# Performance work log

Measured on AMD Instinct MI355X. Metric: run time of the kernel, lower is better.

## Reference

```python
import jax, jax.numpy as jnp
import numpy as np

D_MODEL = 512
D_STATE = 64
SEQ_LEN = 8192
BATCH = 8
LN_EPS = 1e-3  # keras LayerNormalization default epsilon
DELTA_MIN = 0.001
DELTA_MAX = 0.8 * (2.0 / D_STATE)  # default when use_hippo_init=True


def setup_inputs() -> dict:
    key = jax.random.key(0)
    ks = jax.random.split(key, 10)
    x = jax.random.normal(ks[0], (BATCH, SEQ_LEN, D_MODEL), dtype=jnp.float32)
    # Dense layers: glorot-uniform-ish init via scaled normal for simplicity
    def dense_w(k, fan_in, fan_out):
        lim = np.sqrt(6.0 / (fan_in + fan_out))
        return jax.random.uniform(k, (fan_in, fan_out), minval=-lim, maxval=lim, dtype=jnp.float32)
    W_in = dense_w(ks[1], D_MODEL, D_MODEL)
    b_in = jnp.zeros((D_MODEL,), jnp.float32)
    W_xs = dense_w(ks[2], D_MODEL, D_STATE)
    # HiPPO-LegS log init: A_log = log(n+1)
    A_log = jnp.log(jnp.arange(1, D_STATE + 1, dtype=jnp.float32))
    log_delta = jax.random.uniform(ks[3], (D_STATE,), minval=np.log(DELTA_MIN), maxval=np.log(DELTA_MAX), dtype=jnp.float32)
    B = jnp.ones((D_STATE,), jnp.float32)
    C = jax.random.normal(ks[4], (D_STATE,), dtype=jnp.float32)  # stddev=1.0
    D = jnp.ones((D_MODEL,), jnp.float32)
    W_so = dense_w(ks[5], D_STATE, D_MODEL)
    W_out = dense_w(ks[6], D_MODEL, D_MODEL)
    b_out = jnp.zeros((D_MODEL,), jnp.float32)
    ln_gamma = jnp.ones((D_MODEL,), jnp.float32)
    ln_beta = jnp.zeros((D_MODEL,), jnp.float32)
    return {
        "x": x, "ln_gamma": ln_gamma, "ln_beta": ln_beta,
        "W_in": W_in, "b_in": b_in, "W_xs": W_xs,
        "A_log": A_log, "log_delta": log_delta, "B": B, "C": C, "D": D,
        "W_so": W_so, "W_out": W_out, "b_out": b_out,
    }


def reference(x, ln_gamma, ln_beta, W_in, b_in, W_xs, A_log, log_delta, B, C, D, W_so, W_out, b_out):
    Bsz, L, dm = x.shape
    n_fft = 1 << int(np.ceil(np.log2(2 * L - 1)))
    residual = x
    # LayerNorm over last axis (keras default)
    mu = jnp.mean(x, axis=-1, keepdims=True)
    var = jnp.mean(jnp.square(x - mu), axis=-1, keepdims=True)
    xn = (x - mu) * jax.lax.rsqrt(var + LN_EPS) * ln_gamma + ln_beta
    z = xn @ W_in + b_in                       # (B, L, d_model)
    x_state = z @ W_xs                          # (B, L, d_state)
    # Diagonal SSM discretization (bilinear/Tustin)
    A = -jnp.exp(A_log)
    delta = jax.nn.softplus(log_delta)
    dA2 = delta * A / 2.0
    A_bar = (1.0 + dA2) / (1.0 - dA2)           # (d_state,)
    B_bar = delta / (1.0 - dA2) * B             # (d_state,)
    t = jnp.arange(L, dtype=jnp.float32)
    kernel = jnp.power(A_bar[None, :], t[:, None]) * B_bar[None, :]  # (L, d_state)
    # FFT convolution along time
    u_t = jnp.transpose(x_state, (0, 2, 1))     # (B, d_state, L)
    k_t = kernel.T                              # (d_state, L)
    u_f = jnp.fft.rfft(u_t, n=n_fft, axis=-1)
    k_f = jnp.fft.rfft(k_t, n=n_fft, axis=-1)
    y = jnp.fft.irfft(u_f * k_f[None, :, :], n=n_fft, axis=-1)[:, :, :L]
    y_state = jnp.transpose(y, (0, 2, 1))       # (B, L, d_state)
    y_state = y_state * C[None, None, :]
    y = y_state @ W_so                          # (B, L, d_model)
    y = y + D * z
    y = y @ W_out + b_out
    return y + residual
```

## Files before the change

kernel.cpp:

```cpp
#include <hip/hip_runtime.h>
#include <hip/hip_bf16.h>
#include <cstddef>
#include <cstdint>

#define DM 512
#define DS 64
#define L_SEQ 8192
#define NB 8
#define M_ROWS (NB * L_SEQ)
#define LN_EPS 1e-3f
#define NCHUNK 256
#define LCH 32

typedef __attribute__((ext_vector_type(8))) short short8;
typedef __attribute__((ext_vector_type(4))) float f32x4;
using bf16 = __hip_bfloat16;
using ushort_t = unsigned short;

__device__ __forceinline__ unsigned short f2bf(float f) {
    bf16 h = __float2bfloat16(f);
    return *reinterpret_cast<unsigned short*>(&h);
}

__device__ __forceinline__ int swzcol(int row, int col) {
    return (col & ~63) | (((((col >> 3) & 7) ^ (row & 7))) << 3) | (col & 7);
}

__device__ __forceinline__ size_t pkidx(int k, int n, int Kd32) {
    int n16 = n >> 4, fr = n & 15, kt = k >> 5, fq = (k >> 3) & 3, e = k & 7;
    return (((size_t)(n16 * Kd32 + kt) * 64 + fq * 16 + fr) << 3) + e;
}

__device__ __forceinline__ void gload_lds16(const void* g, void* l) {
    __builtin_amdgcn_global_load_lds(
        (const __attribute__((address_space(1))) void*)g,
        (__attribute__((address_space(3))) void*)l, 16, 0, 0);
}

template<int N> __device__ __forceinline__ void wait_vm() {
    static_assert(N == 0 || N == 6, "");
    if constexpr (N == 0) asm volatile("s_waitcnt vmcnt(0)" ::: "memory");
    else                  asm volatile("s_waitcnt vmcnt(6)" ::: "memory");
}

__device__ __forceinline__ void block_barrier() {
    asm volatile("" ::: "memory");
    __builtin_amdgcn_s_barrier();
    asm volatile("" ::: "memory");
}

__global__ __launch_bounds__(256) void prep(const float* __restrict__ W_so,
                                            const float* __restrict__ W_out,
                                            const float* __restrict__ W_in,
                                            const float* __restrict__ W_xs,
                                            const float* __restrict__ b_in,
                                            float* __restrict__ sWsoOut,
                                            float* __restrict__ sWinxs,
                                            float* __restrict__ sBxs)
{
    int i = blockIdx.x * 256 + threadIdx.x;
    if (i < 32768) {
        int s = i >> 9, j = i & 511;
        float a = 0.f;
        for (int c = 0; c < 512; ++c) a += W_so[s * 512 + c] * W_out[c * 512 + j];
        sWsoOut[i] = a;
    } else if (i < 65536) {
        int idx = i - 32768; int k = idx >> 6, n = idx & 63;
        float a = 0.f;
        for (int c = 0; c < 512; ++c) a += W_in[k * 512 + c] * W_xs[c * 64 + n];
        sWinxs[idx] = a;
    } else if (i < 65600) {
        int n = i - 65536;
        float a = 0.f;
        for (int c = 0; c < 512; ++c) a += b_in[c] * W_xs[c * 64 + n];
        sBxs[n] = a;
    }
}

__global__ __launch_bounds__(256) void pack_all(const float* __restrict__ W_in,
                                                const float* __restrict__ sWinxs,
                                                const float* __restrict__ sWsoOut,
                                                const float* __restrict__ W_out,
                                                const float* __restrict__ Dv,
                                                ushort_t* __restrict__ WinPk,
                                                ushort_t* __restrict__ WinxsPk,
                                                ushort_t* __restrict__ WsooutPk,
                                                ushort_t* __restrict__ WdoutPk)
{
    int i = blockIdx.x * 256 + threadIdx.x;
    if (i < 262144) {
        int k = i >> 9, n = i & 511;
        WinPk[pkidx(k, n, 16)] = f2bf(W_in[i]);
    } else if (i < 294912) {
        int j = i - 262144; int k = j >> 6, n = j & 63;
        WinxsPk[pkidx(k, n, 16)] = f2bf(sWinxs[j]);
    } else if (i < 327680) {
        int j = i - 294912; int s = j >> 9, n = j & 511;
        WsooutPk[pkidx(s, n, 2)] = f2bf(sWsoOut[j]);
    } else if (i < 589824) {
        int j = i - 327680; int c = j >> 9, n = j & 511;
        WdoutPk[pkidx(c, n, 16)] = f2bf(Dv[c] * W_out[j]);
    }
}

__global__ __launch_bounds__(64) void ln_kernel(const float* __restrict__ x,
                                                const float* __restrict__ gamma,
                                                const float* __restrict__ beta,
                                                ushort_t* __restrict__ xn)
{
    size_t row = blockIdx.x;
    int lane = threadIdx.x;
    const float4* xr = (const float4*)(x + row * DM);
    float4 v0 = xr[lane * 2];
    float4 v1 = xr[lane * 2 + 1];
    float s  = v0.x + v0.y + v0.z + v0.w + v1.x + v1.y + v1.z + v1.w;
    float s2 = v0.x*v0.x + v0.y*v0.y + v0.z*v0.z + v0.w*v0.w
             + v1.x*v1.x + v1.y*v1.y + v1.z*v1.z + v1.w*v1.w;
    #pragma unroll
    for (int off = 32; off > 0; off >>= 1) {
        s  += __shfl_xor(s,  off);
        s2 += __shfl_xor(s2, off);
    }
    float mu  = s * (1.0f / DM);
    float var = s2 * (1.0f / DM) - mu * mu;
    float rs  = rsqrtf(var + LN_EPS);
    const float4* g4 = (const float4*)gamma;
    const float4* b4 = (const float4*)beta;
    float4 g0 = g4[lane * 2], g1 = g4[lane * 2 + 1];
    float4 bb0 = b4[lane * 2], bb1 = b4[lane * 2 + 1];
    short8 o;
    o[0] = (short)f2bf((v0.x - mu) * rs * g0.x + bb0.x);
    o[1] = (short)f2bf((v0.y - mu) * rs * g0.y + bb0.y);
    o[2] = (short)f2bf((v0.z - mu) * rs * g0.z + bb0.z);
    o[3] = (short)f2bf((v0.w - mu) * rs * g0.w + bb0.w);
    o[4] = (short)f2bf((v1.x - mu) * rs * g1.x + bb1.x);
    o[5] = (short)f2bf((v1.y - mu) * rs * g1.y + bb1.y);
    o[6] = (short)f2bf((v1.z - mu) * rs * g1.z + bb1.z);
    o[7] = (short)f2bf((v1.w - mu) * rs * g1.w + bb1.w);
    int g = (lane & 7) ^ ((int)row & 7);
    *(short8*)(xn + row * DM + (lane >> 3) * 64 + g * 8) = o;
}

__device__ __forceinline__ void store_out(float* C, size_t i, float v) { C[i] = v; }
__device__ __forceinline__ void store_out(bf16* C, size_t i, float v)  { C[i] = __float2bfloat16(v); }

template<int BN, int WR, int WC, typename OutT, bool DUAL, bool HB, bool HA, bool SWZO>
__global__ __launch_bounds__(512, 4) void gemm_bp(const ushort_t* __restrict__ A1,
                                                  const ushort_t* __restrict__ B1,
                                                  const ushort_t* __restrict__ A2,
                                                  const ushort_t* __restrict__ B2,
                                                  const float* __restrict__ bias,
                                                  const float* __restrict__ aux,
                                                  OutT* __restrict__ C,
                                                  int M, int N, int K2)
{
    constexpr int BM = 128;
    constexpr int MF = BM / (16 * WR), NF = BN / (16 * WC);
    static_assert(NF == 2, "b ping-pong arrays assume NF==2");
    __shared__ unsigned char LDS[2][BM * 128];

    const int tid = threadIdx.x;
    const int lane = tid & 63, w = tid >> 6;
    const int fr = lane & 15, fq = lane >> 4;
    const int wr = w % WR, wc = w / WR;

    const int ny = N / BN;
    const int per = (int)gridDim.x >> 3;
    const int lg = ((int)blockIdx.x & 7) * per + ((int)blockIdx.x >> 3);
    const size_t bm0 = (size_t)(lg / ny) * BM;
    const int bn0 = (lg % ny) * BN;
    const int nk = (DUAL ? 1 : 0) + K2 / 64;

    f32x4 acc[MF][NF];
    #pragma unroll
    for (int m = 0; m < MF; ++m)
        #pragma unroll
        for (int n = 0; n < NF; ++n)
            acc[m][n] = (f32x4){0.f, 0.f, 0.f, 0.f};

    auto stage = [&](int buf, int t) {
        #pragma unroll
        for (int j = 0; j < 2; ++j) {
            int r = j * 64 + (tid >> 3);
            const ushort_t* src;
            if constexpr (DUAL) {
                if (t == 0) src = A1 + (bm0 + r) * (size_t)64 + (tid & 7) * 8;
                else        src = A2 + (bm0 + r) * (size_t)512 + (size_t)(t - 1) * 64 + (tid & 7) * 8;
            } else {
                src = A2 + (bm0 + r) * (size_t)K2 + (size_t)t * 64 + (tid & 7) * 8;
            }
            gload_lds16(src, &LDS[buf][j * 8192 + w * 1024]);
        }
    };

    auto loadB = [&](short8 (&bb)[2][2], int t) {
        #pragma unroll
        for (int h = 0; h < 2; ++h)
            #pragma unroll
            for (int n = 0; n < NF; ++n) {
                int n16g = (bn0 + wc * (BN / WC) + n * 16) >> 4;
                const ushort_t* p;
                if constexpr (DUAL) {
                    if (t == 0) p = B1 + (((size_t)(n16g * 2 + h) * 64 + lane) << 3);
                    else        p = B2 + (((size_t)(n16g * 16 + (t - 1) * 2 + h) * 64 + lane) << 3);
                } else {
                    p = B2 + (((size_t)(n16g * (K2 / 32) + t * 2 + h) * 64 + lane) << 3);
                }
                bb[h][n] = *(const short8*)p;
            }
    };

    auto compute = [&](int buf, const short8 (&bb)[2][2]) {
        #pragma unroll
        for (int h = 0; h < 2; ++h) {
            short8 af[MF];
            #pragma unroll
            for (int m = 0; m < MF; ++m) {
                int row = wr * (BM / WR) + m * 16 + fr;
                int g = (h * 4 + fq) ^ (row & 7);
                af[m] = *(const short8*)&LDS[buf][row * 128 + g * 16];
            }
            #pragma unroll
            for (int m = 0; m < MF; ++m)
                #pragma unroll
                for (int n = 0; n < NF; ++n)
                    acc[m][n] = __builtin_amdgcn_mfma_f32_16x16x32_bf16(af[m], bb[h][n], acc[m][n], 0, 0, 0);
        }
    };

    short8 bX[2][2], bY[2][2];
    stage(0, 0);
    loadB(bX, 0);
    int buf = 0;
    for (int t = 0; t < nk; t += 2) {
        if (t + 1 < nk) { stage(buf ^ 1, t + 1); loadB(bY, t + 1); }
        __builtin_amdgcn_sched_barrier(0);
        if (t + 1 < nk) wait_vm<6>(); else wait_vm<0>();
        block_barrier();
        compute(buf, bX);
        if (t + 1 < nk) {
            block_barrier();
            buf ^= 1;
            if (t + 2 < nk) { stage(buf ^ 1, t + 2); loadB(bX, t + 2); }
            __builtin_amdgcn_sched_barrier(0);
            if (t + 2 < nk) wait_vm<6>(); else wait_vm<0>();
            block_barrier();
            compute(buf, bY);
            if (t + 2 < nk) { block_barrier(); buf ^= 1; }
        }
    }

    #pragma unroll
    for (int n = 0; n < NF; ++n) {
        int coll = wc * (BN / WC) + n * 16 + fr;
        int colg = bn0 + coll;
        float bv = HB ? bias[colg] : 0.f;
        #pragma unroll
        for (int m = 0; m < MF; ++m) {
            int rowl = wr * (BM / WR) + m * 16 + fq * 4;
            #pragma unroll
            for (int r = 0; r < 4; ++r) {
                size_t row = bm0 + rowl + r;
                float v = acc[m][n][r] + bv;
                if constexpr (HA) v += aux[row * (size_t)N + colg];
                size_t oc = SWZO ? (size_t)swzcol(rowl + r, colg) : (size_t)colg;
                store_out(C, row * (size_t)N + oc, v);
            }
        }
    }
}

__device__ __forceinline__ void ssm_params(const float* A_log, const float* log_delta,
                                           const float* Bv, int n, float& Ab, float& Bb)
{
    float A  = -expf(A_log[n]);
    float dl = log1pf(expf(log_delta[n]));
    float dA2 = dl * A * 0.5f;
    float inv = 1.0f / (1.0f - dA2);
    Ab = (1.0f + dA2) * inv;
    Bb = dl * inv * Bv[n];
}

__global__ __launch_bounds__(64) void scan_pass1(const float* __restrict__ xs,
                                                 const float* __restrict__ A_log,
                                                 const float* __restrict__ log_delta,
                                                 const float* __restrict__ Bv,
                                                 float* __restrict__ carry)
{
    int b = blockIdx.x / NCHUNK;
    int c = blockIdx.x % NCHUNK;
    int n = threadIdx.x;
    float Ab, Bb;
    ssm_params(A_log, log_delta, Bv, n, Ab, Bb);
    size_t base = ((size_t)b * L_SEQ + (size_t)c * LCH) * DS + n;
    float h = 0.0f;
    for (int t = 0; t < LCH; ++t)
        h = Ab * h + Bb * xs[base + (size_t)t * DS];
    carry[((size_t)b * NCHUNK + c) * DS + n] = h;
}

__global__ __launch_bounds__(64) void scan_pass2(const float* __restrict__ A_log,
                                                 const float* __restrict__ log_delta,
                                                 const float* __restrict__ Bv,
                                                 const float* __restrict__ carry,
                                                 float* __restrict__ hin)
{
    int b = blockIdx.x;
    int n = threadIdx.x;
    float Ab, Bb;
    ssm_params(A_log, log_delta, Bv, n, Ab, Bb);
    float powA = powf(Ab, (float)LCH);
    float h = 0.0f;
    for (int c = 0; c < NCHUNK; ++c) {
        size_t idx = ((size_t)b * NCHUNK + c) * DS + n;
        hin[idx] = h;
        h = powA * h + carry[idx];
    }
}

__global__ __launch_bounds__(64) void scan_pass3(const float* __restrict__ xs,
                                                 const float* __restrict__ A_log,
                                                 const float* __restrict__ log_delta,
                                                 const float* __restrict__ Bv,
                                                 const float* __restrict__ Cv,
                                                 const float* __restrict__ hin,
                                                 ushort_t* __restrict__ ys)
{
    int b = blockIdx.x / NCHUNK;
    int c = blockIdx.x % NCHUNK;
    int n = threadIdx.x;
    float Ab, Bb;
    ssm_params(A_log, log_delta, Bv, n, Ab, Bb);
    float Cn = Cv[n];
    size_t base = ((size_t)b * L_SEQ + (size_t)c * LCH) * DS + n;
    size_t rowbase = ((size_t)b * L_SEQ + (size_t)c * LCH) * DS;
    float h = hin[((size_t)b * NCHUNK + c) * DS + n];
    for (int t = 0; t < LCH; ++t) {
        h = Ab * h + Bb * xs[base + (size_t)t * DS];
        int col = (((n >> 3) ^ (t & 7)) << 3) | (n & 7);
        ys[rowbase + (size_t)t * DS + col] = f2bf(Cn * h);
    }
}

extern "C" void kernel_launch(void* const* d_in, const int* in_sizes, int n_in,
                              void* d_out, int out_size, void* d_ws, size_t ws_size,
                              hipStream_t stream)
{
    const float* x         = (const float*)d_in[0];
    const float* ln_gamma  = (const float*)d_in[1];
    const float* ln_beta   = (const float*)d_in[2];
    const float* W_in      = (const float*)d_in[3];
    const float* b_in      = (const float*)d_in[4];
    const float* W_xs      = (const float*)d_in[5];
    const float* A_log     = (const float*)d_in[6];
    const float* log_delta = (const float*)d_in[7];
    const float* Bv        = (const float*)d_in[8];
    const float* Cv        = (const float*)d_in[9];
    const float* Dv        = (const float*)d_in[10];
    const float* W_so      = (const float*)d_in[11];
    const float* W_out     = (const float*)d_in[12];
    const float* b_out     = (const float*)d_in[13];
    float* out = (float*)d_out;

    const size_t M = M_ROWS;
    float*    xs_f     = (float*)d_ws;
    ushort_t* xn_b     = (ushort_t*)(xs_f + M * DS);
    ushort_t* z_b      = xn_b + M * (size_t)DM;
    ushort_t* ys_b     = z_b + M * (size_t)DM;
    ushort_t* WinPk    = ys_b + M * (size_t)DS;
    ushort_t* WinxsPk  = WinPk + (size_t)DM * DM;
    ushort_t* WsooutPk = WinxsPk + (size_t)DM * DS;
    ushort_t* WdoutPk  = WsooutPk + (size_t)DS * DM;
    float*    sWsoOut  = (float*)(WdoutPk + (size_t)DM * DM);
    float*    sWinxs   = sWsoOut + (size_t)DS * DM;
    float*    sBxs     = sWinxs + (size_t)DM * DS;
    float*    carry    = sBxs + 64;
    float*    hin      = carry + NB * NCHUNK * DS;

    prep<<<dim3(257), dim3(256), 0, stream>>>(W_so, W_out, W_in, W_xs, b_in,
                                              sWsoOut, sWinxs, sBxs);
    pack_all<<<dim3(589824 / 256), dim3(256), 0, stream>>>(W_in, sWinxs, sWsoOut, W_out, Dv,
                                                           WinPk, WinxsPk, WsooutPk, WdoutPk);
    ln_kernel<<<dim3((unsigned)M), dim3(64), 0, stream>>>(x, ln_gamma, ln_beta, xn_b);
    gemm_bp<128, 2, 4, bf16, false, true, false, true>
        <<<dim3((M / 128) * (DM / 128)), dim3(512), 0, stream>>>(nullptr, nullptr, xn_b, WinPk,
                                                                 b_in, nullptr, (bf16*)z_b,
                                                                 (int)M, DM, DM);
    gemm_bp<64, 4, 2, float, false, true, false, false>
        <<<dim3(M / 128), dim3(512), 0, stream>>>(nullptr, nullptr, xn_b, WinxsPk,
                                                  sBxs, nullptr, xs_f, (int)M, DS, DM);
    scan_pass1<<<dim3(NB * NCHUNK), dim3(64), 0, stream>>>(xs_f, A_log, log_delta, Bv, carry);
    scan_pass2<<<dim3(NB), dim3(64), 0, stream>>>(A_log, log_delta, Bv, carry, hin);
    scan_pass3<<<dim3(NB * NCHUNK), dim3(64), 0, stream>>>(xs_f, A_log, log_delta, Bv, Cv, hin, ys_b);
    gemm_bp<128, 2, 4, float, true, true, true, false>
        <<<dim3((M / 128) * (DM / 128)), dim3(512), 0, stream>>>(ys_b, WsooutPk, z_b, WdoutPk,
                                                                 b_out, x, out, (int)M, DM, DM);
}
```

Before: 259.0 us.

## Fold W_in·diag(D)·W_out into one weight, drop the z GEMM and its buffer

Precomputes W_in·diag(D)·W_out and a combined bias so the final GEMM reads the normalized input directly rather than the intermediate z. This removes the full M×512×512 input-projection GEMM and the bf16 write and read of z. In exchange, the prep kernel gains a per-call 512×512×512 weight product on naive scalar loops, plus extra bf16 rounding of the fused weights.

```diff
diff --git a/kernel.cpp b/kernel.cpp
--- a/kernel.cpp
+++ b/kernel.cpp
@@ -54,52 +54,60 @@
                                             const float* __restrict__ W_in,
                                             const float* __restrict__ W_xs,
                                             const float* __restrict__ b_in,
-                                            float* __restrict__ sWsoOut,
-                                            float* __restrict__ sWinxs,
-                                            float* __restrict__ sBxs)
+                                            const float* __restrict__ b_out,
+                                            const float* __restrict__ Dv,
+                                            float* __restrict__ sWc2,
+                                            float* __restrict__ sWc1,
+                                            float* __restrict__ bc1,
+                                            float* __restrict__ sWc3,
+                                            float* __restrict__ bc2)
 {
     int i = blockIdx.x * 256 + threadIdx.x;
     if (i < 32768) {
         int s = i >> 9, j = i & 511;
         float a = 0.f;
         for (int c = 0; c < 512; ++c) a += W_so[s * 512 + c] * W_out[c * 512 + j];
-        sWsoOut[i] = a;
+        sWc2[i] = a;
     } else if (i < 65536) {
         int idx = i - 32768; int k = idx >> 6, n = idx & 63;
         float a = 0.f;
         for (int c = 0; c < 512; ++c) a += W_in[k * 512 + c] * W_xs[c * 64 + n];
-        sWinxs[idx] = a;
+        sWc1[idx] = a;
     } else if (i < 65600) {
         int n = i - 65536;
         float a = 0.f;
         for (int c = 0; c < 512; ++c) a += b_in[c] * W_xs[c * 64 + n];
-        sBxs[n] = a;
-    }
-}
-
-__global__ __launch_bounds__(256) void pack_all(const float* __restrict__ W_in,
-                                                const float* __restrict__ sWinxs,
-                                                const float* __restrict__ sWsoOut,
-                                                const float* __restrict__ W_out,
-                                                const float* __restrict__ Dv,
-                                                ushort_t* __restrict__ WinPk,
-                                                ushort_t* __restrict__ WinxsPk,
-                                                ushort_t* __restrict__ WsooutPk,
-                                                ushort_t* __restrict__ WdoutPk)
+        bc1[n] = a;
+    } else if (i < 327744) {
+        int idx = i - 65600; int k = idx >> 9, j = idx & 511;
+        float a = 0.f;
+        for (int c = 0; c < 512; ++c) a += W_in[k * 512 + c] * Dv[c] * W_out[c * 512 + j];
+        sWc3[idx] = a;
+    } else if (i < 328256) {
+        int j = i - 327744;
+        float a = b_out[j];
+        for (int c = 0; c < 512; ++c) a += b_in[c] * Dv[c] * W_out[c * 512 + j];
+        bc2[j] = a;
+    }
+}
+
+__global__ __launch_bounds__(256) void pack_all(const float* __restrict__ sWc3,
+                                                const float* __restrict__ sWc1,
+                                                const float* __restrict__ sWc2,
+                                                ushort_t* __restrict__ Wc3Pk,
+                                                ushort_t* __restrict__ Wc1Pk,
+                                                ushort_t* __restrict__ Wc2Pk)
 {
     int i = blockIdx.x * 256 + threadIdx.x;
     if (i < 262144) {
         int k = i >> 9, n = i & 511;
-        WinPk[pkidx(k, n, 16)] = f2bf(W_in[i]);
+        Wc3Pk[pkidx(k, n, 16)] = f2bf(sWc3[i]);
     } else if (i < 294912) {
         int j = i - 262144; int k = j >> 6, n = j & 63;
-        WinxsPk[pkidx(k, n, 16)] = f2bf(sWinxs[j]);
+        Wc1Pk[pkidx(k, n, 16)] = f2bf(sWc1[j]);
     } else if (i < 327680) {
         int j = i - 294912; int s = j >> 9, n = j & 511;
-        WsooutPk[pkidx(s, n, 2)] = f2bf(sWsoOut[j]);
-    } else if (i < 589824) {
-        int j = i - 327680; int c = j >> 9, n = j & 511;
-        WdoutPk[pkidx(c, n, 16)] = f2bf(Dv[c] * W_out[j]);
+        Wc2Pk[pkidx(s, n, 2)] = f2bf(sWc2[j]);
     }
 }
 
@@ -363,36 +371,31 @@
     float* out = (float*)d_out;
 
     const size_t M = M_ROWS;
-    float*    xs_f     = (float*)d_ws;
-    ushort_t* xn_b     = (ushort_t*)(xs_f + M * DS);
-    ushort_t* z_b      = xn_b + M * (size_t)DM;
-    ushort_t* ys_b     = z_b + M * (size_t)DM;
-    ushort_t* WinPk    = ys_b + M * (size_t)DS;
-    ushort_t* WinxsPk  = WinPk + (size_t)DM * DM;
-    ushort_t* WsooutPk = WinxsPk + (size_t)DM * DS;
-    ushort_t* WdoutPk  = WsooutPk + (size_t)DS * DM;
-    float*    sWsoOut  = (float*)(WdoutPk + (size_t)DM * DM);
-    float*    sWinxs   = sWsoOut + (size_t)DS * DM;
-    float*    sBxs     = sWinxs + (size_t)DM * DS;
-    float*    carry    = sBxs + 64;
-    float*    hin      = carry + NB * NCHUNK * DS;
-
-    prep<<<dim3(257), dim3(256), 0, stream>>>(W_so, W_out, W_in, W_xs, b_in,
-                                              sWsoOut, sWinxs, sBxs);
-    pack_all<<<dim3(589824 / 256), dim3(256), 0, stream>>>(W_in, sWinxs, sWsoOut, W_out, Dv,
-                                                           WinPk, WinxsPk, WsooutPk, WdoutPk);
+    float*    xs_f   = (float*)d_ws;
+    ushort_t* xn_b   = (ushort_t*)(xs_f + M * DS);
+    ushort_t* ys_b   = xn_b + M * (size_t)DM;
+    ushort_t* Wc3Pk  = ys_b + M * (size_t)DS;
+    ushort_t* Wc1Pk  = Wc3Pk + (size_t)DM * DM;
+    ushort_t* Wc2Pk  = Wc1Pk + (size_t)DM * DS;
+    float*    sWc2   = (float*)(Wc2Pk + (size_t)DS * DM);
+    float*    sWc1   = sWc2 + (size_t)DS * DM;
+    float*    bc1    = sWc1 + (size_t)DM * DS;
+    float*    sWc3   = bc1 + 64;
+    float*    bc2    = sWc3 + (size_t)DM * DM;
+    float*    carry  = bc2 + DM;
+    float*    hin    = carry + NB * NCHUNK * DS;
+
+    prep<<<dim3(1283), dim3(256), 0, stream>>>(W_so, W_out, W_in, W_xs, b_in, b_out, Dv,
+                                               sWc2, sWc1, bc1, sWc3, bc2);
+    pack_all<<<dim3(1280), dim3(256), 0, stream>>>(sWc3, sWc1, sWc2, Wc3Pk, Wc1Pk, Wc2Pk);
     ln_kernel<<<dim3((unsigned)M), dim3(64), 0, stream>>>(x, ln_gamma, ln_beta, xn_b);
-    gemm_bp<128, 2, 4, bf16, false, true, false, true>
-        <<<dim3((M / 128) * (DM / 128)), dim3(512), 0, stream>>>(nullptr, nullptr, xn_b, WinPk,
-                                                                 b_in, nullptr, (bf16*)z_b,
-                                                                 (int)M, DM, DM);
     gemm_bp<64, 4, 2, float, false, true, false, false>
-        <<<dim3(M / 128), dim3(512), 0, stream>>>(nullptr, nullptr, xn_b, WinxsPk,
-                                                  sBxs, nullptr, xs_f, (int)M, DS, DM);
+        <<<dim3(M / 128), dim3(512), 0, stream>>>(nullptr, nullptr, xn_b, Wc1Pk,
+                                                  bc1, nullptr, xs_f, (int)M, DS, DM);
     scan_pass1<<<dim3(NB * NCHUNK), dim3(64), 0, stream>>>(xs_f, A_log, log_delta, Bv, carry);
     scan_pass2<<<dim3(NB), dim3(64), 0, stream>>>(A_log, log_delta, Bv, carry, hin);
     scan_pass3<<<dim3(NB * NCHUNK), dim3(64), 0, stream>>>(xs_f, A_log, log_delta, Bv, Cv, hin, ys_b);
     gemm_bp<128, 2, 4, float, true, true, true, false>
-        <<<dim3((M / 128) * (DM / 128)), dim3(512), 0, stream>>>(ys_b, WsooutPk, z_b, WdoutPk,
-                                                                 b_out, x, out, (int)M, DM, DM);
-}
+        <<<dim3((M / 128) * (DM / 128)), dim3(512), 0, stream>>>(ys_b, Wc2Pk, xn_b, Wc3Pk,
+                                                                 bc2, x, out, (int)M, DM, DM);
+}
```

Measured after the change: 211.7 us. 1.22x faster.
